# Kernel tuning notes

Measured on AMD Instinct MI355X. Metric: run time of the kernel, lower is better.

The kernel has to match this reference:

```python
import jax, jax.numpy as jnp
import numpy as np

B, T, C, H = 4, 1024, 1024, 16
DH = C // H  # 64


def l1_cdist(a, b, chunk):
    """L1 pairwise distances. a: [..., M, D], b: [..., N, D] -> [..., M, N].
    Scans over feature-dim chunks to avoid a [..., M, N, D] blowup."""
    D = a.shape[-1]
    nc = D // chunk
    a_r = jnp.moveaxis(a.reshape(a.shape[:-1] + (nc, chunk)), -2, 0)  # [nc, ..., M, c]
    b_r = jnp.moveaxis(b.reshape(b.shape[:-1] + (nc, chunk)), -2, 0)  # [nc, ..., N, c]
    init = jnp.zeros(jnp.broadcast_shapes(a.shape[:-2], b.shape[:-2]) + (a.shape[-2], b.shape[-2]), a.dtype)
    def step(acc, ab):
        ac, bc = ab
        return acc + jnp.abs(ac[..., :, None, :] - bc[..., None, :, :]).sum(-1), None
    return jax.lax.scan(step, init, (a_r, b_r))[0]


def sq_cdist(a, b):
    """Squared L2 pairwise distances via GEMM. a: [..., M, D], b: [..., N, D]."""
    aa = jnp.sum(a * a, -1)[..., :, None]
    bb = jnp.sum(b * b, -1)[..., None, :]
    ab = jnp.einsum('...md,...nd->...mn', a, b)
    return jnp.maximum(aa + bb - 2.0 * ab, 0.0)


def delta_linear(x, W, gain):
    """ProxyDeltaLinear: distance-based linear projection. x: [B,T,Din], W: [Dout,Din], gain: [Dout]."""
    Bx, Tx, Din = x.shape
    xa = jnp.tanh(x).reshape(-1, Din)          # [B*T, Din]
    wa = jnp.tanh(W)                           # [Dout, Din]
    l1m = jax.lax.stop_gradient(l1_cdist(xa, wa, 16)) / Din
    l2m = sq_cdist(xa, wa) / Din
    # straight-through: forward value uses l1_mean, gradient flows through l2_sq_mean
    dist = jax.lax.stop_gradient(l1m - l2m) + l2m
    out = (1.0 - dist).reshape(Bx, Tx, -1)
    return (out - 0.5) * gain                  # gain broadcasts over last dim


def reference(x, wq_w, wq_gain, wk_w, wk_gain, wv_w, wv_gain, wo_w, wo_b, gamma, rho):
    q = delta_linear(x, wq_w, wq_gain).reshape(B, T, H, DH).transpose(0, 2, 1, 3)  # [B,H,T,DH]
    k = delta_linear(x, wk_w, wk_gain).reshape(B, T, H, DH).transpose(0, 2, 1, 3)
    v = delta_linear(x, wv_w, wv_gain).reshape(B, T, H, DH).transpose(0, 2, 1, 3)

    l1m = jax.lax.stop_gradient(l1_cdist(q, k, 2)) / DH   # [B,H,T,T]
    l2m = sq_cdist(q, k) / DH
    dist = jax.lax.stop_gradient(l1m - l2m) + l2m

    g = jax.nn.softplus(gamma).reshape(1, H, 1, 1) + 1e-4
    r = jax.nn.softplus(rho).reshape(1, H, 1, 1) + 1e-4
    base = 1.0 / (1.0 + g * dist)
    w = base ** r
    probs = w / (jnp.sum(w, -1, keepdims=True) + 1e-6)

    out = jnp.einsum('bhqk,bhkd->bhqd', probs, v)         # [B,H,T,DH]
    out = out.transpose(0, 2, 1, 3).reshape(B, T, C)
    return out @ wo_w.T + wo_b


def setup_inputs():
    key = jax.random.key(0)
    ks = jax.random.split(key, 5)
    p = lambda kk, shape: jax.random.normal(kk, shape, jnp.float32) * 0.02
    return {
        "x": jax.random.normal(ks[0], (B, T, C), jnp.float32),
        "wq_w": p(ks[1], (C, C)), "wq_gain": jnp.full((C,), 2.0, jnp.float32),
        "wk_w": p(ks[2], (C, C)), "wk_gain": jnp.full((C,), 2.0, jnp.float32),
        "wv_w": p(ks[3], (C, C)), "wv_gain": jnp.full((C,), 2.0, jnp.float32),
        "wo_w": p(ks[4], (C, C)), "wo_b": jnp.zeros((C,), jnp.float32),
        "gamma": jnp.ones((H,), jnp.float32), "rho": jnp.full((H,), 2.0, jnp.float32),
    }
```

## Files before the change

### kernel.cpp

```cpp
#include <hip/hip_runtime.h>
#include <math.h>

namespace {
constexpr int NB  = 4;
constexpr int NT  = 1024;
constexpr int NC  = 1024;
constexpr int NH  = 16;
constexpr int MT  = NB * NT;
}

typedef _Float16 f16x8 __attribute__((ext_vector_type(8)));
typedef float f32x4 __attribute__((ext_vector_type(4)));
typedef int i32x4 __attribute__((ext_vector_type(4)));

__device__ __forceinline__ unsigned sad8(unsigned a, unsigned b, unsigned c) {
  unsigned d;
  asm("v_sad_u8 %0, %1, %2, %3" : "=v"(d) : "v"(a), "v"(b), "v"(c));
  return d;
}

__device__ __forceinline__ float rlog2(float x) {
  float r; asm("v_log_f32 %0, %1" : "=v"(r) : "v"(x)); return r;
}
__device__ __forceinline__ float rexp2(float x) {
  float r; asm("v_exp_f32 %0, %1" : "=v"(r) : "v"(x)); return r;
}
__device__ __forceinline__ unsigned pk16(float a, float b) {
  auto h = __builtin_amdgcn_cvt_pkrtz(a, b);
  return __builtin_bit_cast(unsigned, h);
}

__device__ __forceinline__ unsigned short f16u(float x) {
  _Float16 h = (_Float16)x;
  return __builtin_bit_cast(unsigned short, h);
}

__global__ __launch_bounds__(256) void k_prep(const float* __restrict__ x,
                                              const float* __restrict__ wq,
                                              const float* __restrict__ wk,
                                              const float* __restrict__ wv,
                                              const float* __restrict__ wo,
                                              unsigned* __restrict__ sgnx,
                                              unsigned* __restrict__ wi8,
                                              float* __restrict__ sumax,
                                              unsigned short* __restrict__ woh) {
  const int bid = blockIdx.x;
  const int tid = threadIdx.x;
  if (bid < 2048) {
    int i8o = bid * 256 + tid;
    const float4* in4 = reinterpret_cast<const float4*>(x);
    float4 v0 = in4[2 * i8o], v1 = in4[2 * i8o + 1];
    float t[8] = {v0.x, v0.y, v0.z, v0.w, v1.x, v1.y, v1.z, v1.w};
    unsigned b[8];
    float s = 0.0f;
#pragma unroll
    for (int j = 0; j < 8; ++j) {
      float tv = tanhf(t[j]);
      s += fabsf(tv);
      b[j] = (tv >= 0.0f) ? 0x01u : 0xFFu;
    }
    uint2 o = {b[0] | (b[1] << 8) | (b[2] << 16) | (b[3] << 24),
               b[4] | (b[5] << 8) | (b[6] << 16) | (b[7] << 24)};
    reinterpret_cast<uint2*>(sgnx)[i8o] = o;
#pragma unroll
    for (int off = 32; off > 0; off >>= 1) s += __shfl_down(s, off, 64);
    __shared__ float ws[4];
    if ((tid & 63) == 0) ws[tid >> 6] = s;
    __syncthreads();
    if (tid == 0) {
      sumax[2 * bid]     = ws[0] + ws[1];
      sumax[2 * bid + 1] = ws[2] + ws[3];
    }
  } else if (bid < 3584) {
    const float* in;
    int local;
    if (bid < 2560)      { in = wq; local = bid - 2048; }
    else if (bid < 3072) { in = wk; local = bid - 2560; }
    else                 { in = wv; local = bid - 3072; }
    unsigned* out = wi8 + ((bid < 2560) ? 0 : (bid < 3072) ? (1024 * 256) : (2048 * 256));
    int i8o = local * 256 + tid;
    const float4* in4 = reinterpret_cast<const float4*>(in);
    float4 v0 = in4[2 * i8o], v1 = in4[2 * i8o + 1];
    float t[8] = {v0.x, v0.y, v0.z, v0.w, v1.x, v1.y, v1.z, v1.w};
    unsigned q[8];
#pragma unroll
    for (int j = 0; j < 8; ++j) {
      int qi = __float2int_rn(tanhf(t[j]) * 1024.0f);
      q[j] = (unsigned)qi & 255u;
    }
    uint2 o = {q[0] | (q[1] << 8) | (q[2] << 16) | (q[3] << 24),
               q[4] | (q[5] << 8) | (q[6] << 16) | (q[7] << 24)};
    reinterpret_cast<uint2*>(out)[i8o] = o;
  } else {
    int i = (bid - 3584) * 256 + tid;
    const float4* in4 = reinterpret_cast<const float4*>(wo);
    float4 v0 = in4[2 * i], v1 = in4[2 * i + 1];
    ushort4 o0 = {f16u(v0.x), f16u(v0.y), f16u(v0.z), f16u(v0.w)};
    ushort4 o1 = {f16u(v1.x), f16u(v1.y), f16u(v1.z), f16u(v1.w)};
    reinterpret_cast<ushort4*>(woh)[2 * i] = o0;
    reinterpret_cast<ushort4*>(woh)[2 * i + 1] = o1;
  }
}

__global__ __launch_bounds__(256, 2) void k_signproj(const unsigned* __restrict__ sgnx,
                                                     const unsigned* __restrict__ wi8,
                                                     const float* __restrict__ sumax,
                                                     const float* __restrict__ g0,
                                                     const float* __restrict__ g1,
                                                     const float* __restrict__ g2,
                                                     unsigned* __restrict__ qq,
                                                     unsigned* __restrict__ kq,
                                                     unsigned short* __restrict__ vh) {
  __shared__ unsigned Ash[128][36];
  __shared__ unsigned Bsh[128][36];

  const int tid = threadIdx.x;
  const int n0 = blockIdx.x * 128;
  const int m0 = blockIdx.y * 128;
  const int lane = tid & 63;
  const int wvI = tid >> 6;
  const int wr = wvI >> 1, wc = wvI & 1;
  const int lr = lane & 15, lq = lane >> 4;

  i32x4 acc[4][4] = {};

  const unsigned* A = sgnx + (size_t)m0 * 256;
  const unsigned* Bm = wi8 + (size_t)n0 * 256;

  for (int ks = 0; ks < 8; ++ks) {
    __syncthreads();
#pragma unroll
    for (int p = 0; p < 4; ++p) {
      int idx = tid + p * 256;
      int r = idx >> 3;
      int q4 = (idx & 7) * 4;
      *reinterpret_cast<uint4*>(&Ash[r][q4]) =
          *reinterpret_cast<const uint4*>(A + (size_t)r * 256 + ks * 32 + q4);
      *reinterpret_cast<uint4*>(&Bsh[r][q4]) =
          *reinterpret_cast<const uint4*>(Bm + (size_t)r * 256 + ks * 32 + q4);
    }
    __syncthreads();

#pragma unroll
    for (int kk = 0; kk < 2; ++kk) {
      i32x4 af[4], bf[4];
#pragma unroll
      for (int f = 0; f < 4; ++f) {
        uint4 au = *reinterpret_cast<const uint4*>(&Ash[wr * 64 + f * 16 + lr][kk * 16 + lq * 4]);
        af[f] = __builtin_bit_cast(i32x4, au);
        uint4 bu = *reinterpret_cast<const uint4*>(&Bsh[wc * 64 + f * 16 + lr][kk * 16 + lq * 4]);
        bf[f] = __builtin_bit_cast(i32x4, bu);
      }
#pragma unroll
      for (int fm = 0; fm < 4; ++fm)
#pragma unroll
        for (int fn = 0; fn < 4; ++fn)
          acc[fm][fn] = __builtin_amdgcn_mfma_i32_16x16x64_i8(af[fm], bf[fn], acc[fm][fn], 0, 0, 0);
    }
  }

  const int z = n0 >> 10;
  const int nloc = n0 & 1023;
  const int hl = nloc >> 6;
  const int bI = m0 >> 10;
  const int tloc0 = (m0 & 1023) + wr * 64;
  const float* G = (z == 0) ? g0 : ((z == 1) ? g1 : g2);
  const int h = hl + wc;

  float sx[4][4];
#pragma unroll
  for (int fm = 0; fm < 4; ++fm) {
    float4 sv = *reinterpret_cast<const float4*>(sumax + m0 + wr * 64 + fm * 16 + lq * 4);
    sx[fm][0] = sv.x; sx[fm][1] = sv.y; sx[fm][2] = sv.z; sx[fm][3] = sv.w;
  }

  if (z < 2) {
    unsigned* dst = (z == 0) ? qq : kq;
    const int sh = (lr & 3) * 8;
#pragma unroll
    for (int fn = 0; fn < 4; ++fn) {
      float gn = G[nloc + wc * 64 + fn * 16 + lr];
      int txw = (fn * 16 + lr) >> 2;
#pragma unroll
      for (int fm = 0; fm < 4; ++fm) {
#pragma unroll
        for (int reg = 0; reg < 4; ++reg) {
          float accf = (float)acc[fm][fn][reg];
          float dist = (sx[fm][reg] - accf * (1.0f / 1024.0f)) * (1.0f / 1024.0f);
          float val = (0.5f - dist) * gn;
          unsigned p = ((unsigned)fminf(fmaxf(fmaf(val, 64.0f, 128.5f), 0.0f), 255.0f)) << sh;
          p |= __shfl_xor(p, 1, 64);
          p |= __shfl_xor(p, 2, 64);
          if ((lr & 3) == 0) {
            int t = tloc0 + fm * 16 + lq * 4 + reg;
            dst[(((size_t)(bI * NH + h)) * NT + t) * 16 + txw] = p;
          }
        }
      }
    }
  } else {
#pragma unroll
    for (int fn = 0; fn < 4; ++fn) {
      int dh = fn * 16 + lr;
      float gn = G[nloc + wc * 64 + dh];
#pragma unroll
      for (int fm = 0; fm < 4; ++fm) {
        int t0 = tloc0 + fm * 16 + lq * 4;
        ushort4 o;
#pragma unroll
        for (int reg = 0; reg < 4; ++reg) {
          float accf = (float)acc[fm][fn][reg];
          float dist = (sx[fm][reg] - accf * (1.0f / 1024.0f)) * (1.0f / 1024.0f);
          float val = (0.5f - dist) * gn;
          ((unsigned short*)&o)[reg] = f16u(val);
        }
        *reinterpret_cast<ushort4*>(vh + ((size_t)(bI * NH + h) * 64 + dh) * NT + t0) = o;
      }
    }
  }
}

__global__ __launch_bounds__(512, 4) void k_attn7(const unsigned* __restrict__ qq,
                                                  const unsigned* __restrict__ kq,
                                                  const unsigned short* __restrict__ vh,
                                                  const float* __restrict__ gamma,
                                                  const float* __restrict__ rho,
                                                  unsigned short* __restrict__ att_h) {
  const int qt = blockIdx.x;
  const int h  = blockIdx.y;
  const int b  = blockIdx.z;

  __shared__ unsigned Qs[16][132];
  __shared__ unsigned Ks[16][132];
  __shared__ unsigned Vt[64][68];
  __shared__ unsigned Ws[128][72];
  __shared__ float Inv[128];

  const int tid = threadIdx.x;
  const int lane = tid & 63;
  const int lr = lane & 15, lq = lane >> 4;
  const int w16 = (tid >> 6) * 16;
  const int ty = tid >> 5;
  const int tx = tid & 31;

  const float g  = log1pf(expf(gamma[h])) + 1e-4f;
  const float rr = log1pf(expf(rho[h])) + 1e-4f;
  const float gs = g * (1.0f / (64.0f * 64.0f));
  const float nrr = -rr;

  const unsigned* qbase = qq + (((size_t)(b * NH + h)) * NT + qt * 128) * 16;
  {
    int r = tid >> 2;
    int c4 = (tid & 3) * 4;
    uint4 v = *reinterpret_cast<const uint4*>(qbase + (size_t)r * 16 + c4);
    Qs[c4 + 0][r] = v.x; Qs[c4 + 1][r] = v.y;
    Qs[c4 + 2][r] = v.z; Qs[c4 + 3][r] = v.w;
  }

  f32x4 acc[4] = {};
  float wsum[8] = {0.f, 0.f, 0.f, 0.f, 0.f, 0.f, 0.f, 0.f};

  const unsigned* kbh = kq + (((size_t)(b * NH + h)) * NT) * 16;
  const unsigned* v32 = reinterpret_cast<const unsigned*>(vh + ((size_t)(b * NH + h) * 64) * NT);

  for (int kt = 0; kt < 8; ++kt) {
    __syncthreads();
    {
      const unsigned* kbase = kbh + (size_t)(kt * 128) * 16;
      int r = tid >> 2;
      int c4 = (tid & 3) * 4;
      uint4 v = *reinterpret_cast<const uint4*>(kbase + (size_t)r * 16 + c4);
      int cc = ((r & 7) < 4) ? ((r >> 3) * 4 + (r & 3)) : (64 + (r >> 3) * 4 + (r & 3));
      Ks[c4 + 0][cc] = v.x; Ks[c4 + 1][cc] = v.y;
      Ks[c4 + 2][cc] = v.z; Ks[c4 + 3][cc] = v.w;
    }
#pragma unroll
    for (int p = 0; p < 2; ++p) {
      int idx = tid + p * 512;
      int d = idx >> 4;
      int q4 = (idx & 15) * 4;
      uint4 v = *reinterpret_cast<const uint4*>(v32 + (size_t)d * 512 + kt * 64 + q4);
      *reinterpret_cast<uint4*>(&Vt[d][q4]) = v;
    }
    __syncthreads();

    const int kbase_col = ((tx & 1) << 6) + (tx >> 1) * 4;
    unsigned dl[8][4] = {};
#pragma unroll 8
    for (int du = 0; du < 16; ++du) {
      uint4 q0 = *reinterpret_cast<const uint4*>(&Qs[du][ty * 8]);
      uint4 q1 = *reinterpret_cast<const uint4*>(&Qs[du][ty * 8 + 4]);
      uint4 kv = *reinterpret_cast<const uint4*>(&Ks[du][kbase_col]);
      unsigned qa[8] = {q0.x, q0.y, q0.z, q0.w, q1.x, q1.y, q1.z, q1.w};
      unsigned ka[4] = {kv.x, kv.y, kv.z, kv.w};
#pragma unroll
      for (int i = 0; i < 8; ++i)
#pragma unroll
        for (int j = 0; j < 4; ++j) dl[i][j] = sad8(qa[i], ka[j], dl[i][j]);
    }

#pragma unroll
    for (int i = 0; i < 8; ++i) {
      int qrow = ty * 8 + i;
      float w0[4];
#pragma unroll
      for (int j = 0; j < 4; ++j)
        w0[j] = rexp2(nrr * rlog2(fmaf(gs, (float)dl[i][j], 1.0f)));
      wsum[i] += (w0[0] + w0[1]) + (w0[2] + w0[3]);
      uint2 pk = {pk16(w0[0], w0[1]), pk16(w0[2], w0[3])};
      *reinterpret_cast<uint2*>(&Ws[qrow][(tx * 2) ^ ((qrow & 1) << 2)]) = pk;
    }
    __syncthreads();

#pragma unroll
    for (int kk = 0; kk < 4; ++kk) {
      int r = w16 + lr;
      uint4 au = *reinterpret_cast<const uint4*>(&Ws[r][(kk * 16 + lq * 4) ^ ((r & 1) << 2)]);
      f16x8 af = __builtin_bit_cast(f16x8, au);
#pragma unroll
      for (int nt = 0; nt < 4; ++nt) {
        uint4 bu = *reinterpret_cast<const uint4*>(&Vt[nt * 16 + lr][kk * 16 + lq * 4]);
        f16x8 bf = __builtin_bit_cast(f16x8, bu);
        acc[nt] = __builtin_amdgcn_mfma_f32_16x16x32_f16(af, bf, acc[nt], 0, 0, 0);
      }
    }
  }

#pragma unroll
  for (int i = 0; i < 8; ++i) {
    float s = wsum[i];
    s += __shfl_xor(s, 1, 64);
    s += __shfl_xor(s, 2, 64);
    s += __shfl_xor(s, 4, 64);
    s += __shfl_xor(s, 8, 64);
    s += __shfl_xor(s, 16, 64);
    if (tx == 0) Inv[ty * 8 + i] = 1.0f / (s + 1e-6f);
  }
  __syncthreads();

  {
    float iv[4];
#pragma unroll
    for (int r = 0; r < 4; ++r) iv[r] = Inv[w16 + lq * 4 + r];
    const size_t rowbase = (size_t)(b * NT + qt * 128 + w16 + lq * 4);
    const int colbase = h * 64 + lr;
#pragma unroll
    for (int nt = 0; nt < 4; ++nt)
#pragma unroll
      for (int r = 0; r < 4; ++r)
        att_h[(rowbase + r) * NC + colbase + nt * 16] = f16u(acc[nt][r] * iv[r]);
  }
}

__global__ __launch_bounds__(256) void k_gemm16(const unsigned short* __restrict__ A,
                                                const unsigned short* __restrict__ Bw,
                                                const float* __restrict__ bias,
                                                float* __restrict__ Out) {
  __shared__ unsigned Ash[128 * 20];
  __shared__ unsigned Bsh[128 * 20];

  const int tid = threadIdx.x;
  const int m0 = blockIdx.y * 128;
  const int n0 = blockIdx.x * 128;
  const int lane = tid & 63;
  const int wv = tid >> 6;
  const int wr = wv >> 1, wc = wv & 1;
  const int lr = lane & 15, lq = lane >> 4;

  f32x4 acc[4][4] = {};

  const unsigned* A32 = reinterpret_cast<const unsigned*>(A);
  const unsigned* B32 = reinterpret_cast<const unsigned*>(Bw);

  for (int ks = 0; ks < 32; ++ks) {
    __syncthreads();
#pragma unroll
    for (int p = 0; p < 2; ++p) {
      int idx = tid + p * 256;
      int r = idx >> 2, q = idx & 3;
      uint4 av = *reinterpret_cast<const uint4*>(A32 + (size_t)(m0 + r) * 512 + ks * 16 + q * 4);
      *reinterpret_cast<uint4*>(&Ash[r * 20 + q * 4]) = av;
      uint4 bv = *reinterpret_cast<const uint4*>(B32 + (size_t)(n0 + r) * 512 + ks * 16 + q * 4);
      *reinterpret_cast<uint4*>(&Bsh[r * 20 + q * 4]) = bv;
    }
    __syncthreads();

    f16x8 af[4], bf[4];
#pragma unroll
    for (int f = 0; f < 4; ++f) {
      uint4 au = *reinterpret_cast<const uint4*>(&Ash[(wr * 64 + f * 16 + lr) * 20 + lq * 4]);
      af[f] = __builtin_bit_cast(f16x8, au);
      uint4 bu = *reinterpret_cast<const uint4*>(&Bsh[(wc * 64 + f * 16 + lr) * 20 + lq * 4]);
      bf[f] = __builtin_bit_cast(f16x8, bu);
    }
#pragma unroll
    for (int fm = 0; fm < 4; ++fm)
#pragma unroll
      for (int fn = 0; fn < 4; ++fn)
        acc[fm][fn] = __builtin_amdgcn_mfma_f32_16x16x32_f16(af[fm], bf[fn], acc[fm][fn], 0, 0, 0);
  }

#pragma unroll
  for (int fn = 0; fn < 4; ++fn) {
    int col = n0 + wc * 64 + fn * 16 + lr;
    float bb = bias[col];
#pragma unroll
    for (int fm = 0; fm < 4; ++fm) {
      int rowb = m0 + wr * 64 + fm * 16 + lq * 4;
#pragma unroll
      for (int r = 0; r < 4; ++r)
        Out[(size_t)(rowb + r) * NC + col] = acc[fm][fn][r] + bb;
    }
  }
}

extern "C" void kernel_launch(void* const* d_in, const int* in_sizes, int n_in,
                              void* d_out, int out_size, void* d_ws, size_t ws_size,
                              hipStream_t stream) {
  (void)in_sizes; (void)n_in; (void)out_size; (void)ws_size;
  const float* x     = (const float*)d_in[0];
  const float* wq_w  = (const float*)d_in[1];
  const float* wq_g  = (const float*)d_in[2];
  const float* wk_w  = (const float*)d_in[3];
  const float* wk_g  = (const float*)d_in[4];
  const float* wv_w  = (const float*)d_in[5];
  const float* wv_g  = (const float*)d_in[6];
  const float* wo_w  = (const float*)d_in[7];
  const float* wo_b  = (const float*)d_in[8];
  const float* gamma = (const float*)d_in[9];
  const float* rho   = (const float*)d_in[10];
  float* out = (float*)d_out;

  unsigned* sgnx = (unsigned*)d_ws;
  unsigned* wi8  = sgnx + (size_t)MT * 256;
  float* sumax   = (float*)(wi8 + 3072ull * 256);
  unsigned* qqhm = (unsigned*)(sumax + MT);
  unsigned* kqhm = qqhm + (size_t)NB * NH * NT * 16;
  unsigned short* vhdm = (unsigned short*)(kqhm + (size_t)NB * NH * NT * 16);
  unsigned short* atth = vhdm + (size_t)NB * NH * 64 * NT;
  unsigned short* woh  = atth + (size_t)MT * NC;

  k_prep<<<4096, 256, 0, stream>>>(x, wq_w, wk_w, wv_w, wo_w, sgnx, wi8, sumax, woh);

  k_signproj<<<dim3(3072 / 128, MT / 128), 256, 0, stream>>>(sgnx, wi8, sumax,
                                                             wq_g, wk_g, wv_g,
                                                             qqhm, kqhm, vhdm);

  k_attn7<<<dim3(NT / 128, NH, NB), 512, 0, stream>>>(qqhm, kqhm, vhdm, gamma, rho, atth);

  k_gemm16<<<dim3(NC / 128, MT / 128, 1), 256, 0, stream>>>(atth, woh, wo_b, out);
}
```

Measured before the change: 126.4 us.

## Drop LDS staging in projection and output GEMMs, load MFMA fragments directly

Both the int8 sign-projection GEMM and the f16 output GEMM stop staging tiles through shared memory. Each wave now loads its MFMA operand fragments straight from global memory, which removes the two barriers per K-step. The output GEMM also shrinks its tile to 64x128 so there are twice as many blocks, and both kernels raise their occupancy hints. The tradeoff is redundant global and L2 traffic, since waves no longer share loaded tiles, and uncoalesced 16-byte row-strided loads.

```diff
diff --git a/kernel.cpp b/kernel.cpp
--- a/kernel.cpp
+++ b/kernel.cpp
@@ -102,7 +102,7 @@
   }
 }
 
-__global__ __launch_bounds__(256, 2) void k_signproj(const unsigned* __restrict__ sgnx,
+__global__ __launch_bounds__(256, 3) void k_signproj(const unsigned* __restrict__ sgnx,
                                                      const unsigned* __restrict__ wi8,
                                                      const float* __restrict__ sumax,
                                                      const float* __restrict__ g0,
@@ -111,9 +111,6 @@
                                                      unsigned* __restrict__ qq,
                                                      unsigned* __restrict__ kq,
                                                      unsigned short* __restrict__ vh) {
-  __shared__ unsigned Ash[128][36];
-  __shared__ unsigned Bsh[128][36];
-
   const int tid = threadIdx.x;
   const int n0 = blockIdx.x * 128;
   const int m0 = blockIdx.y * 128;
@@ -124,32 +121,19 @@
 
   i32x4 acc[4][4] = {};
 
-  const unsigned* A = sgnx + (size_t)m0 * 256;
-  const unsigned* Bm = wi8 + (size_t)n0 * 256;
+  const unsigned* Arow0 = sgnx + (size_t)(m0 + wr * 64 + lr) * 256 + lq * 4;
+  const unsigned* Brow0 = wi8  + (size_t)(n0 + wc * 64 + lr) * 256 + lq * 4;
 
   for (int ks = 0; ks < 8; ++ks) {
-    __syncthreads();
-#pragma unroll
-    for (int p = 0; p < 4; ++p) {
-      int idx = tid + p * 256;
-      int r = idx >> 3;
-      int q4 = (idx & 7) * 4;
-      *reinterpret_cast<uint4*>(&Ash[r][q4]) =
-          *reinterpret_cast<const uint4*>(A + (size_t)r * 256 + ks * 32 + q4);
-      *reinterpret_cast<uint4*>(&Bsh[r][q4]) =
-          *reinterpret_cast<const uint4*>(Bm + (size_t)r * 256 + ks * 32 + q4);
-    }
-    __syncthreads();
-
 #pragma unroll
     for (int kk = 0; kk < 2; ++kk) {
       i32x4 af[4], bf[4];
 #pragma unroll
       for (int f = 0; f < 4; ++f) {
-        uint4 au = *reinterpret_cast<const uint4*>(&Ash[wr * 64 + f * 16 + lr][kk * 16 + lq * 4]);
-        af[f] = __builtin_bit_cast(i32x4, au);
-        uint4 bu = *reinterpret_cast<const uint4*>(&Bsh[wc * 64 + f * 16 + lr][kk * 16 + lq * 4]);
-        bf[f] = __builtin_bit_cast(i32x4, bu);
+        af[f] = __builtin_bit_cast(i32x4,
+            *reinterpret_cast<const uint4*>(Arow0 + (size_t)f * 16 * 256 + ks * 32 + kk * 16));
+        bf[f] = __builtin_bit_cast(i32x4,
+            *reinterpret_cast<const uint4*>(Brow0 + (size_t)f * 16 * 256 + ks * 32 + kk * 16));
       }
 #pragma unroll
       for (int fm = 0; fm < 4; ++fm)
@@ -352,61 +336,49 @@
   }
 }
 
-__global__ __launch_bounds__(256) void k_gemm16(const unsigned short* __restrict__ A,
-                                                const unsigned short* __restrict__ Bw,
-                                                const float* __restrict__ bias,
-                                                float* __restrict__ Out) {
-  __shared__ unsigned Ash[128 * 20];
-  __shared__ unsigned Bsh[128 * 20];
-
+__global__ __launch_bounds__(256, 2) void k_gemm16(const unsigned short* __restrict__ A,
+                                                   const unsigned short* __restrict__ Bw,
+                                                   const float* __restrict__ bias,
+                                                   float* __restrict__ Out) {
   const int tid = threadIdx.x;
-  const int m0 = blockIdx.y * 128;
   const int n0 = blockIdx.x * 128;
+  const int m0 = blockIdx.y * 64;
   const int lane = tid & 63;
-  const int wv = tid >> 6;
-  const int wr = wv >> 1, wc = wv & 1;
+  const int wvI = tid >> 6;
   const int lr = lane & 15, lq = lane >> 4;
 
-  f32x4 acc[4][4] = {};
+  f32x4 acc[4][2] = {};
 
   const unsigned* A32 = reinterpret_cast<const unsigned*>(A);
   const unsigned* B32 = reinterpret_cast<const unsigned*>(Bw);
-
+  const unsigned* Arow0 = A32 + (size_t)(m0 + lr) * 512 + lq * 4;
+  const unsigned* Brow0 = B32 + (size_t)(n0 + wvI * 32 + lr) * 512 + lq * 4;
+
+#pragma unroll 2
   for (int ks = 0; ks < 32; ++ks) {
-    __syncthreads();
-#pragma unroll
-    for (int p = 0; p < 2; ++p) {
-      int idx = tid + p * 256;
-      int r = idx >> 2, q = idx & 3;
-      uint4 av = *reinterpret_cast<const uint4*>(A32 + (size_t)(m0 + r) * 512 + ks * 16 + q * 4);
-      *reinterpret_cast<uint4*>(&Ash[r * 20 + q * 4]) = av;
-      uint4 bv = *reinterpret_cast<const uint4*>(B32 + (size_t)(n0 + r) * 512 + ks * 16 + q * 4);
-      *reinterpret_cast<uint4*>(&Bsh[r * 20 + q * 4]) = bv;
-    }
-    __syncthreads();
-
-    f16x8 af[4], bf[4];
-#pragma unroll
-    for (int f = 0; f < 4; ++f) {
-      uint4 au = *reinterpret_cast<const uint4*>(&Ash[(wr * 64 + f * 16 + lr) * 20 + lq * 4]);
-      af[f] = __builtin_bit_cast(f16x8, au);
-      uint4 bu = *reinterpret_cast<const uint4*>(&Bsh[(wc * 64 + f * 16 + lr) * 20 + lq * 4]);
-      bf[f] = __builtin_bit_cast(f16x8, bu);
-    }
+    f16x8 af[4], bf[2];
 #pragma unroll
     for (int fm = 0; fm < 4; ++fm)
-#pragma unroll
-      for (int fn = 0; fn < 4; ++fn)
+      af[fm] = __builtin_bit_cast(f16x8,
+          *reinterpret_cast<const uint4*>(Arow0 + (size_t)fm * 16 * 512 + ks * 16));
+#pragma unroll
+    for (int fn = 0; fn < 2; ++fn)
+      bf[fn] = __builtin_bit_cast(f16x8,
+          *reinterpret_cast<const uint4*>(Brow0 + (size_t)fn * 16 * 512 + ks * 16));
+#pragma unroll
+    for (int fm = 0; fm < 4; ++fm)
+#pragma unroll
+      for (int fn = 0; fn < 2; ++fn)
         acc[fm][fn] = __builtin_amdgcn_mfma_f32_16x16x32_f16(af[fm], bf[fn], acc[fm][fn], 0, 0, 0);
   }
 
 #pragma unroll
-  for (int fn = 0; fn < 4; ++fn) {
-    int col = n0 + wc * 64 + fn * 16 + lr;
+  for (int fn = 0; fn < 2; ++fn) {
+    int col = n0 + wvI * 32 + fn * 16 + lr;
     float bb = bias[col];
 #pragma unroll
     for (int fm = 0; fm < 4; ++fm) {
-      int rowb = m0 + wr * 64 + fm * 16 + lq * 4;
+      int rowb = m0 + fm * 16 + lq * 4;
 #pragma unroll
       for (int r = 0; r < 4; ++r)
         Out[(size_t)(rowb + r) * NC + col] = acc[fm][fn][r] + bb;
@@ -448,5 +420,5 @@
 
   k_attn7<<<dim3(NT / 128, NH, NB), 512, 0, stream>>>(qqhm, kqhm, vhdm, gamma, rho, atth);
 
-  k_gemm16<<<dim3(NC / 128, MT / 128, 1), 256, 0, stream>>>(atth, woh, wo_b, out);
-}
+  k_gemm16<<<dim3(NC / 128, MT / 64), 256, 0, stream>>>(atth, woh, wo_b, out);
+}
```

Result: slower. 175.5 us (+38.9%).
